# Optimization experiments

Hardware: AMD Instinct MI355X
Metric: run time of the kernel (lower is better)

## Reference

```python
import jax, jax.numpy as jnp
import numpy as np
import math

B, S, D = 2, 2048, 2048
P = 4       # num_entangled_pairs
PW = 2      # num_interference_pathways
L = 2       # num_layers
STD = 0.02
EPS = 1e-5


def _layer_norm(x, g, b):
    m = jnp.mean(x, axis=-1, keepdims=True)
    v = jnp.mean(jnp.square(x - m), axis=-1, keepdims=True)
    return (x - m) * jax.lax.rsqrt(v + EPS) * g + b


def setup_inputs() -> dict:
    key = jax.random.key(0)
    ks = jax.random.split(key, 16)
    n = lambda k, shape: jax.random.normal(k, shape, dtype=jnp.float32) * STD
    inp = {
        "x": jax.random.normal(ks[0], (B, S, D), dtype=jnp.float32),
        # superposition layer
        "amp_w": n(ks[1], (D, D)), "amp_b": jnp.zeros((D,), jnp.float32),
        "ph_w": n(ks[2], (D, D)), "ph_b": jnp.zeros((D,), jnp.float32),
        # per-layer entanglement
        "ent_w": n(ks[3], (L, D, P * D)), "ent_b": jnp.zeros((L, P * D), jnp.float32),
        "ent_pw": n(ks[4], (L, P * D, D)), "ent_pb": jnp.zeros((L, D), jnp.float32),
        # per-layer interference pathways
        "path_w": n(ks[5], (L, PW, D, D)), "path_b": jnp.zeros((L, PW, D), jnp.float32),
        "phase": jax.random.normal(ks[6], (L, PW, D), dtype=jnp.float32),
        # layer norms (norm3 / norm4 of each layer)
        "ln3_g": jnp.ones((L, D), jnp.float32), "ln3_b": jnp.zeros((L, D), jnp.float32),
        "ln4_g": jnp.ones((L, D), jnp.float32), "ln4_b": jnp.zeros((L, D), jnp.float32),
    }
    return inp


def reference(x, amp_w, amp_b, ph_w, ph_b, ent_w, ent_b, ent_pw, ent_pb,
              path_w, path_b, phase, ln3_g, ln3_b, ln4_g, ln4_b):
    # QuantumSuperpositionLayer on the input
    amp = jax.nn.sigmoid(x @ amp_w + amp_b)
    ph = jnp.tanh(x @ ph_w + ph_b) * math.pi
    h = (jnp.cos(ph) + jnp.sin(ph)) * amp                      # [B,S,D]

    for l in range(L):
        # QuantumEntanglementLayer: expand to P*D then project back
        e = h @ ent_w[l] + ent_b[l]                            # [B,S,P*D]
        ent = e @ ent_pw[l] + ent_pb[l]                        # [B,S,D]
        h = _layer_norm(h + ent, ln3_g[l], ln3_b[l])

        # QuantumInterferenceLayer: sum over pathways with phase modulation
        t = jnp.einsum('bsd,pdf->pbsf', h, path_w[l]) + path_b[l][:, None, None, :]
        mod = jnp.cos(phase[l]) + jnp.sin(phase[l])            # [PW,D]
        interf = jnp.sum(t * mod[:, None, None, :], axis=0)   # [B,S,D]
        h = _layer_norm(h + interf, ln4_g[l], ln4_b[l])
    return h
```

## Files before the change

### kernel.cpp

```cpp
#include <hip/hip_runtime.h>
#include <cstdint>
#include <cstddef>

typedef unsigned short u16;
typedef short bf16x8 __attribute__((ext_vector_type(8)));
typedef float f32x4 __attribute__((ext_vector_type(4)));

__device__ __forceinline__ float bf2f(u16 v) {
  union { unsigned int u; float f; } x; x.u = ((unsigned int)v) << 16; return x.f;
}
__device__ __forceinline__ u16 f2bf(float f) {
  union { float f; unsigned int u; } x; x.f = f;
  unsigned int r = (x.u + 0x7fffu + ((x.u >> 16) & 1u)) >> 16;
  return (u16)r;
}

__device__ __forceinline__ void async16(const u16* g, u16* lds) {
  __builtin_amdgcn_global_load_lds(
      (const __attribute__((address_space(1))) void*)g,
      (__attribute__((address_space(3))) void*)lds, 16, 0, 0);
}

#define BM 128
#define BN 128
#define BK 64

__global__ __launch_bounds__(256) void gemm_bt(
    const u16* __restrict__ A, const u16* __restrict__ Bt,
    const float* __restrict__ bias, u16* __restrict__ C,
    int M, int N, int K)
{
  __shared__ __align__(16) u16 As[BM * BK];
  __shared__ __align__(16) u16 Bs[BN * BK];
  const int tid = threadIdx.x;
  const int w   = tid >> 6;
  const int l   = tid & 63;
  const int bm  = blockIdx.x;
  const int bn  = blockIdx.y;
  const int wm  = w >> 1;
  const int wn  = w & 1;
  const int tRow = l & 15;
  const int quad = l >> 4;

  const u16* ag[4]; const u16* bg[4];
  u16* al[4]; u16* bl[4];
  #pragma unroll
  for (int i = 0; i < 4; ++i) {
    int s = i * 4 + w;
    int row = s * 8 + (l >> 3);
    ag[i] = A  + (size_t)(bm * BM + row) * K + (l & 7) * 8;
    bg[i] = Bt + (size_t)(bn * BN + row) * K + (l & 7) * 8;
    al[i] = &As[s * 512];
    bl[i] = &Bs[s * 512];
  }

  f32x4 acc[4][4] = {};

  for (int k0 = 0; k0 < K; k0 += BK) {
    __syncthreads();
    #pragma unroll
    for (int i = 0; i < 4; ++i) {
      async16(ag[i], al[i]);
      async16(bg[i], bl[i]);
      ag[i] += BK; bg[i] += BK;
    }
    __syncthreads();
    #pragma unroll
    for (int ks = 0; ks < BK; ks += 32) {
      bf16x8 af[4], bfr[4];
      #pragma unroll
      for (int mt = 0; mt < 4; ++mt)
        af[mt] = *(const bf16x8*)&As[(wm * 64 + mt * 16 + tRow) * BK + ks + quad * 8];
      #pragma unroll
      for (int nt = 0; nt < 4; ++nt)
        bfr[nt] = *(const bf16x8*)&Bs[(wn * 64 + nt * 16 + tRow) * BK + ks + quad * 8];
      #pragma unroll
      for (int mt = 0; mt < 4; ++mt)
        #pragma unroll
        for (int nt = 0; nt < 4; ++nt)
          acc[mt][nt] = __builtin_amdgcn_mfma_f32_16x16x32_bf16(af[mt], bfr[nt], acc[mt][nt], 0, 0, 0);
    }
  }

  const int crow0 = bm * BM + wm * 64;
  const int ccol0 = bn * BN + wn * 64;
  #pragma unroll
  for (int nt = 0; nt < 4; ++nt) {
    int col = ccol0 + nt * 16 + tRow;
    float bv = bias[col];
    #pragma unroll
    for (int mt = 0; mt < 4; ++mt) {
      int r0 = crow0 + mt * 16 + quad * 4;
      #pragma unroll
      for (int r = 0; r < 4; ++r)
        C[(size_t)(r0 + r) * N + col] = f2bf(acc[mt][nt][r] + bv);
    }
  }
}

__global__ __launch_bounds__(256) void transpose_f2bf(
    const float* __restrict__ src, u16* __restrict__ dst, int R, int C)
{
  __shared__ __align__(16) u16 tile[64][72];
  const int bx = blockIdx.x;
  const int by = blockIdx.y;
  const int t = threadIdx.x;
  const int r  = t >> 4;
  const int c4 = (t & 15) * 4;
  #pragma unroll
  for (int i = 0; i < 4; ++i) {
    int row = r + i * 16;
    f32x4 v = *(const f32x4*)&src[(size_t)(by * 64 + row) * C + bx * 64 + c4];
    #pragma unroll
    for (int j = 0; j < 4; ++j) tile[row][c4 + j] = f2bf(v[j]);
  }
  __syncthreads();
  const int orow0 = t >> 3;
  const int oc8   = (t & 7) * 8;
  #pragma unroll
  for (int i = 0; i < 2; ++i) {
    int orow = orow0 + i * 32;
    u16 tmp[8];
    #pragma unroll
    for (int j = 0; j < 8; ++j) tmp[j] = tile[oc8 + j][orow];
    *(uint4*)&dst[(size_t)(bx * 64 + orow) * R + by * 64 + oc8] = *(uint4*)tmp;
  }
}

__global__ void cvt_f2bf(const float* __restrict__ s, u16* __restrict__ d) {
  size_t i = ((size_t)blockIdx.x * 256 + threadIdx.x) * 8;
  f32x4 a = *(const f32x4*)&s[i];
  f32x4 b = *(const f32x4*)&s[i + 4];
  u16 o[8];
  #pragma unroll
  for (int j = 0; j < 4; ++j) { o[j] = f2bf(a[j]); o[j + 4] = f2bf(b[j]); }
  *(uint4*)&d[i] = *(uint4*)o;
}

__global__ void mod_k(const float* __restrict__ ph, float* __restrict__ m, int n) {
  int i = blockIdx.x * 256 + threadIdx.x;
  if (i < n) { float p = ph[i]; m[i] = cosf(p) + sinf(p); }
}

__global__ __launch_bounds__(256) void combine_path_k(
    const float* __restrict__ pw, const float* __restrict__ mod,
    u16* __restrict__ WcT, int D)
{
  __shared__ float tile[64][65];
  const int bx = blockIdx.x;
  const int by = blockIdx.y;
  const int t = threadIdx.x;
  const int r  = t >> 4;
  const int c4 = (t & 15) * 4;
  float acc[4][4];
  #pragma unroll
  for (int i = 0; i < 4; ++i)
    #pragma unroll
    for (int j = 0; j < 4; ++j) acc[i][j] = 0.f;
  for (int p = 0; p < 2; ++p) {
    float m[4];
    #pragma unroll
    for (int j = 0; j < 4; ++j) m[j] = mod[p * D + bx * 64 + c4 + j];
    #pragma unroll
    for (int i = 0; i < 4; ++i) {
      int d = by * 64 + r + i * 16;
      f32x4 v = *(const f32x4*)&pw[((size_t)p * D + d) * D + bx * 64 + c4];
      #pragma unroll
      for (int j = 0; j < 4; ++j) acc[i][j] += v[j] * m[j];
    }
  }
  #pragma unroll
  for (int i = 0; i < 4; ++i)
    #pragma unroll
    for (int j = 0; j < 4; ++j) tile[r + i * 16][c4 + j] = acc[i][j];
  __syncthreads();
  const int fo0 = t >> 3;
  const int oc8 = (t & 7) * 8;
  #pragma unroll
  for (int i = 0; i < 2; ++i) {
    int fo = fo0 + i * 32;
    u16 tmp[8];
    #pragma unroll
    for (int j = 0; j < 8; ++j) tmp[j] = f2bf(tile[oc8 + j][fo]);
    *(uint4*)&WcT[(size_t)(bx * 64 + fo) * D + by * 64 + oc8] = *(uint4*)tmp;
  }
}

__global__ void combine_bias_k(const float* __restrict__ pb, const float* __restrict__ mod,
                               float* __restrict__ bc, int D) {
  int f = blockIdx.x * 256 + threadIdx.x;
  if (f < D) bc[f] = pb[f] * mod[f] + pb[D + f] * mod[D + f];
}

__global__ __launch_bounds__(256) void superpose_k(
    const u16* __restrict__ z1, const u16* __restrict__ z2, u16* __restrict__ h)
{
  size_t i = ((size_t)blockIdx.x * 256 + threadIdx.x) * 8;
  uint4 v1 = *(const uint4*)&z1[i];
  uint4 v2 = *(const uint4*)&z2[i];
  const u16* p1 = (const u16*)&v1;
  const u16* p2 = (const u16*)&v2;
  u16 o[8];
  #pragma unroll
  for (int j = 0; j < 8; ++j) {
    float a = bf2f(p1[j]);
    float p = bf2f(p2[j]);
    float amp = 1.f / (1.f + __expf(-a));
    float ph = 3.14159265358979323f * tanhf(p);
    float s, c;
    __sincosf(ph, &s, &c);
    o[j] = f2bf((c + s) * amp);
  }
  *(uint4*)&h[i] = *(uint4*)o;
}

template <bool F32OUT>
__global__ __launch_bounds__(256) void add_ln_k(
    const u16* __restrict__ hin, const u16* __restrict__ delta,
    const float* __restrict__ g, const float* __restrict__ b,
    void* __restrict__ outp, int D)
{
  const int row = blockIdx.x;
  const int t = threadIdx.x;
  const size_t base = (size_t)row * D;
  uint4 hv = *(const uint4*)&hin[base + t * 8];
  uint4 dv = *(const uint4*)&delta[base + t * 8];
  const u16* hp = (const u16*)&hv;
  const u16* dp = (const u16*)&dv;
  float x[8];
  float s = 0.f, s2 = 0.f;
  #pragma unroll
  for (int j = 0; j < 8; ++j) {
    x[j] = bf2f(hp[j]) + bf2f(dp[j]);
    s += x[j]; s2 += x[j] * x[j];
  }
  #pragma unroll
  for (int o = 32; o > 0; o >>= 1) {
    s  += __shfl_down(s, o, 64);
    s2 += __shfl_down(s2, o, 64);
  }
  __shared__ float ss[4], ss2[4];
  if ((t & 63) == 0) { ss[t >> 6] = s; ss2[t >> 6] = s2; }
  __syncthreads();
  float S  = ss[0] + ss[1] + ss[2] + ss[3];
  float S2 = ss2[0] + ss2[1] + ss2[2] + ss2[3];
  float mean = S / D;
  float var = S2 / D - mean * mean;
  float rstd = rsqrtf(var + 1e-5f);
  float y[8];
  #pragma unroll
  for (int j = 0; j < 8; ++j)
    y[j] = (x[j] - mean) * rstd * g[t * 8 + j] + b[t * 8 + j];
  if constexpr (F32OUT) {
    float* out = (float*)outp;
    f32x4 lo = {y[0], y[1], y[2], y[3]};
    f32x4 hi = {y[4], y[5], y[6], y[7]};
    *(f32x4*)&out[base + t * 8]     = lo;
    *(f32x4*)&out[base + t * 8 + 4] = hi;
  } else {
    u16* out = (u16*)outp;
    u16 o8[8];
    #pragma unroll
    for (int j = 0; j < 8; ++j) o8[j] = f2bf(y[j]);
    *(uint4*)&out[base + t * 8] = *(uint4*)o8;
  }
}

extern "C" void kernel_launch(void* const* d_in, const int* in_sizes, int n_in,
                              void* d_out, int out_size, void* d_ws, size_t ws_size,
                              hipStream_t stream) {
  const float* x      = (const float*)d_in[0];
  const float* amp_w  = (const float*)d_in[1];
  const float* amp_b  = (const float*)d_in[2];
  const float* ph_w   = (const float*)d_in[3];
  const float* ph_b   = (const float*)d_in[4];
  const float* ent_w  = (const float*)d_in[5];
  const float* ent_b  = (const float*)d_in[6];
  const float* ent_pw = (const float*)d_in[7];
  const float* ent_pb = (const float*)d_in[8];
  const float* path_w = (const float*)d_in[9];
  const float* path_b = (const float*)d_in[10];
  const float* phase  = (const float*)d_in[11];
  const float* ln3_g  = (const float*)d_in[12];
  const float* ln3_b  = (const float*)d_in[13];
  const float* ln4_g  = (const float*)d_in[14];
  const float* ln4_b  = (const float*)d_in[15];

  constexpr int D = 2048, PD = 8192, M = 4096, L = 2, PW = 2;

  char* p = (char*)d_ws;
  u16* wT = (u16*)p; p += (size_t)PD * D * sizeof(u16);
  u16* h  = (u16*)p; p += (size_t)M * D * sizeof(u16);
  u16* t1 = (u16*)p; p += (size_t)M * D * sizeof(u16);
  u16* e  = (u16*)p; p += (size_t)M * PD * sizeof(u16);
  float* modf = (float*)p; p += (size_t)L * PW * D * sizeof(float);
  float* bcf  = (float*)p; p += (size_t)D * sizeof(float);

  u16* xb = e;
  u16* z1 = e + (size_t)M * D;
  u16* z2 = e + (size_t)2 * M * D;

  dim3 b256(256);

  mod_k<<<(L * PW * D) / 256, b256, 0, stream>>>(phase, modf, L * PW * D);
  cvt_f2bf<<<(M * D) / (256 * 8), b256, 0, stream>>>(x, xb);

  transpose_f2bf<<<dim3(D / 64, D / 64), b256, 0, stream>>>(amp_w, wT, D, D);
  gemm_bt<<<dim3(M / BM, D / BN), b256, 0, stream>>>(xb, wT, amp_b, z1, M, D, D);
  transpose_f2bf<<<dim3(D / 64, D / 64), b256, 0, stream>>>(ph_w, wT, D, D);
  gemm_bt<<<dim3(M / BM, D / BN), b256, 0, stream>>>(xb, wT, ph_b, z2, M, D, D);
  superpose_k<<<(M * D) / (256 * 8), b256, 0, stream>>>(z1, z2, h);

  for (int l = 0; l < L; ++l) {
    transpose_f2bf<<<dim3(PD / 64, D / 64), b256, 0, stream>>>(ent_w + (size_t)l * D * PD, wT, D, PD);
    gemm_bt<<<dim3(M / BM, PD / BN), b256, 0, stream>>>(h, wT, ent_b + (size_t)l * PD, e, M, PD, D);
    transpose_f2bf<<<dim3(D / 64, PD / 64), b256, 0, stream>>>(ent_pw + (size_t)l * PD * D, wT, PD, D);
    gemm_bt<<<dim3(M / BM, D / BN), b256, 0, stream>>>(e, wT, ent_pb + (size_t)l * D, t1, M, D, PD);
    add_ln_k<false><<<M, b256, 0, stream>>>(h, t1, ln3_g + (size_t)l * D, ln3_b + (size_t)l * D, h, D);
    combine_path_k<<<dim3(D / 64, D / 64), b256, 0, stream>>>(
        path_w + (size_t)l * PW * D * D, modf + (size_t)l * PW * D, wT, D);
    combine_bias_k<<<D / 256, b256, 0, stream>>>(path_b + (size_t)l * PW * D, modf + (size_t)l * PW * D, bcf, D);
    gemm_bt<<<dim3(M / BM, D / BN), b256, 0, stream>>>(h, wT, bcf, t1, M, D, D);
    if (l == L - 1)
      add_ln_k<true><<<M, b256, 0, stream>>>(h, t1, ln4_g + (size_t)l * D, ln4_b + (size_t)l * D, d_out, D);
    else
      add_ln_k<false><<<M, b256, 0, stream>>>(h, t1, ln4_g + (size_t)l * D, ln4_b + (size_t)l * D, h, D);
  }
}
```

Before: 1.402 ms.

## Swizzle GEMM LDS layout, fuse amp/phase GEMMs, split entanglement weights

Adds an XOR swizzle to the LDS tile layout in the GEMM so the MFMA fragment reads avoid bank conflicts. Merges the amplitude and phase projections into one wider GEMM with concatenated weights and biases. Splits the entanglement expand and project GEMMs into halves so the transposed weight buffer is half as large, with the second projection half accumulating into the bf16 output. The split adds launches and a bf16 read-modify-write accumulation step, which costs some precision.

```diff
diff --git a/kernel.cpp b/kernel.cpp
--- a/kernel.cpp
+++ b/kernel.cpp
@@ -25,9 +25,12 @@
 #define BN 128
 #define BK 64
 
+template <bool ACC>
 __global__ __launch_bounds__(256) void gemm_bt(
-    const u16* __restrict__ A, const u16* __restrict__ Bt,
-    const float* __restrict__ bias, u16* __restrict__ C,
+    const u16* __restrict__ A, int lda,
+    const u16* __restrict__ Bt,
+    const float* __restrict__ bias,
+    u16* __restrict__ C, int ldc,
     int M, int N, int K)
 {
   __shared__ __align__(16) u16 As[BM * BK];
@@ -48,8 +51,9 @@
   for (int i = 0; i < 4; ++i) {
     int s = i * 4 + w;
     int row = s * 8 + (l >> 3);
-    ag[i] = A  + (size_t)(bm * BM + row) * K + (l & 7) * 8;
-    bg[i] = Bt + (size_t)(bn * BN + row) * K + (l & 7) * 8;
+    int c   = (l & 7) ^ ((l >> 3) & 7);
+    ag[i] = A  + (size_t)(bm * BM + row) * lda + c * 8;
+    bg[i] = Bt + (size_t)(bn * BN + row) * K   + c * 8;
     al[i] = &As[s * 512];
     bl[i] = &Bs[s * 512];
   }
@@ -67,13 +71,20 @@
     __syncthreads();
     #pragma unroll
     for (int ks = 0; ks < BK; ks += 32) {
+      const int lc = (ks >> 3) + quad;
       bf16x8 af[4], bfr[4];
       #pragma unroll
-      for (int mt = 0; mt < 4; ++mt)
-        af[mt] = *(const bf16x8*)&As[(wm * 64 + mt * 16 + tRow) * BK + ks + quad * 8];
-      #pragma unroll
-      for (int nt = 0; nt < 4; ++nt)
-        bfr[nt] = *(const bf16x8*)&Bs[(wn * 64 + nt * 16 + tRow) * BK + ks + quad * 8];
+      for (int mt = 0; mt < 4; ++mt) {
+        int r = wm * 64 + mt * 16 + tRow;
+        int p = lc ^ (tRow & 7);
+        af[mt] = *(const bf16x8*)&As[r * BK + p * 8];
+      }
+      #pragma unroll
+      for (int nt = 0; nt < 4; ++nt) {
+        int r = wn * 64 + nt * 16 + tRow;
+        int p = lc ^ (tRow & 7);
+        bfr[nt] = *(const bf16x8*)&Bs[r * BK + p * 8];
+      }
       #pragma unroll
       for (int mt = 0; mt < 4; ++mt)
         #pragma unroll
@@ -87,19 +98,24 @@
   #pragma unroll
   for (int nt = 0; nt < 4; ++nt) {
     int col = ccol0 + nt * 16 + tRow;
-    float bv = bias[col];
+    float bv = ACC ? 0.f : bias[col];
     #pragma unroll
     for (int mt = 0; mt < 4; ++mt) {
       int r0 = crow0 + mt * 16 + quad * 4;
       #pragma unroll
-      for (int r = 0; r < 4; ++r)
-        C[(size_t)(r0 + r) * N + col] = f2bf(acc[mt][nt][r] + bv);
+      for (int r = 0; r < 4; ++r) {
+        size_t idx = (size_t)(r0 + r) * ldc + col;
+        float v = acc[mt][nt][r] + bv;
+        if (ACC) v += bf2f(C[idx]);
+        C[idx] = f2bf(v);
+      }
     }
   }
 }
 
 __global__ __launch_bounds__(256) void transpose_f2bf(
-    const float* __restrict__ src, u16* __restrict__ dst, int R, int C)
+    const float* __restrict__ src, u16* __restrict__ dst,
+    int R, int C, int srcStride, int col0)
 {
   __shared__ __align__(16) u16 tile[64][72];
   const int bx = blockIdx.x;
@@ -110,7 +126,7 @@
   #pragma unroll
   for (int i = 0; i < 4; ++i) {
     int row = r + i * 16;
-    f32x4 v = *(const f32x4*)&src[(size_t)(by * 64 + row) * C + bx * 64 + c4];
+    f32x4 v = *(const f32x4*)&src[(size_t)(by * 64 + row) * srcStride + col0 + bx * 64 + c4];
     #pragma unroll
     for (int j = 0; j < 4; ++j) tile[row][c4 + j] = f2bf(v[j]);
   }
@@ -140,6 +156,12 @@
 __global__ void mod_k(const float* __restrict__ ph, float* __restrict__ m, int n) {
   int i = blockIdx.x * 256 + threadIdx.x;
   if (i < n) { float p = ph[i]; m[i] = cosf(p) + sinf(p); }
+}
+
+__global__ void concat2_k(const float* __restrict__ a, const float* __restrict__ b,
+                          float* __restrict__ d, int n) {
+  int i = blockIdx.x * 256 + threadIdx.x;
+  if (i < n) { d[i] = a[i]; d[n + i] = b[i]; }
 }
 
 __global__ __launch_bounds__(256) void combine_path_k(
@@ -193,11 +215,15 @@
 }
 
 __global__ __launch_bounds__(256) void superpose_k(
-    const u16* __restrict__ z1, const u16* __restrict__ z2, u16* __restrict__ h)
-{
-  size_t i = ((size_t)blockIdx.x * 256 + threadIdx.x) * 8;
-  uint4 v1 = *(const uint4*)&z1[i];
-  uint4 v2 = *(const uint4*)&z2[i];
+    const u16* __restrict__ zc, u16* __restrict__ h, int D)
+{
+  size_t idx = (size_t)blockIdx.x * 256 + threadIdx.x;
+  int grpPerRow = D / 8;
+  size_t row = idx / grpPerRow;
+  int cg = (int)(idx % grpPerRow);
+  size_t zbase = row * (size_t)(2 * D) + cg * 8;
+  uint4 v1 = *(const uint4*)&zc[zbase];
+  uint4 v2 = *(const uint4*)&zc[zbase + D];
   const u16* p1 = (const u16*)&v1;
   const u16* p2 = (const u16*)&v2;
   u16 o[8];
@@ -211,7 +237,7 @@
     __sincosf(ph, &s, &c);
     o[j] = f2bf((c + s) * amp);
   }
-  *(uint4*)&h[i] = *(uint4*)o;
+  *(uint4*)&h[row * D + cg * 8] = *(uint4*)o;
 }
 
 template <bool F32OUT>
@@ -287,40 +313,55 @@
   const float* ln4_b  = (const float*)d_in[15];
 
   constexpr int D = 2048, PD = 8192, M = 4096, L = 2, PW = 2;
+  constexpr int HPD = PD / 2;
 
   char* p = (char*)d_ws;
-  u16* wT = (u16*)p; p += (size_t)PD * D * sizeof(u16);
+  float* modf = (float*)p; p += (size_t)L * PW * D * sizeof(float);
+  float* bcf  = (float*)p; p += (size_t)2 * D * sizeof(float);
+  p = (char*)d_ws + 65536;
   u16* h  = (u16*)p; p += (size_t)M * D * sizeof(u16);
   u16* t1 = (u16*)p; p += (size_t)M * D * sizeof(u16);
+  u16* wT = (u16*)p; p += (size_t)HPD * D * sizeof(u16);
   u16* e  = (u16*)p; p += (size_t)M * PD * sizeof(u16);
-  float* modf = (float*)p; p += (size_t)L * PW * D * sizeof(float);
-  float* bcf  = (float*)p; p += (size_t)D * sizeof(float);
 
   u16* xb = e;
-  u16* z1 = e + (size_t)M * D;
-  u16* z2 = e + (size_t)2 * M * D;
+  u16* zc = e + (size_t)M * D;
 
   dim3 b256(256);
 
   mod_k<<<(L * PW * D) / 256, b256, 0, stream>>>(phase, modf, L * PW * D);
   cvt_f2bf<<<(M * D) / (256 * 8), b256, 0, stream>>>(x, xb);
 
-  transpose_f2bf<<<dim3(D / 64, D / 64), b256, 0, stream>>>(amp_w, wT, D, D);
-  gemm_bt<<<dim3(M / BM, D / BN), b256, 0, stream>>>(xb, wT, amp_b, z1, M, D, D);
-  transpose_f2bf<<<dim3(D / 64, D / 64), b256, 0, stream>>>(ph_w, wT, D, D);
-  gemm_bt<<<dim3(M / BM, D / BN), b256, 0, stream>>>(xb, wT, ph_b, z2, M, D, D);
-  superpose_k<<<(M * D) / (256 * 8), b256, 0, stream>>>(z1, z2, h);
+  transpose_f2bf<<<dim3(D / 64, D / 64), b256, 0, stream>>>(amp_w, wT, D, D, D, 0);
+  transpose_f2bf<<<dim3(D / 64, D / 64), b256, 0, stream>>>(ph_w, wT + (size_t)D * D, D, D, D, 0);
+  concat2_k<<<D / 256, b256, 0, stream>>>(amp_b, ph_b, bcf, D);
+  gemm_bt<false><<<dim3(M / BM, (2 * D) / BN), b256, 0, stream>>>(
+      xb, D, wT, bcf, zc, 2 * D, M, 2 * D, D);
+  superpose_k<<<(M * D) / (256 * 8), b256, 0, stream>>>(zc, h, D);
 
   for (int l = 0; l < L; ++l) {
-    transpose_f2bf<<<dim3(PD / 64, D / 64), b256, 0, stream>>>(ent_w + (size_t)l * D * PD, wT, D, PD);
-    gemm_bt<<<dim3(M / BM, PD / BN), b256, 0, stream>>>(h, wT, ent_b + (size_t)l * PD, e, M, PD, D);
-    transpose_f2bf<<<dim3(D / 64, PD / 64), b256, 0, stream>>>(ent_pw + (size_t)l * PD * D, wT, PD, D);
-    gemm_bt<<<dim3(M / BM, D / BN), b256, 0, stream>>>(e, wT, ent_pb + (size_t)l * D, t1, M, D, PD);
+    for (int s = 0; s < 2; ++s) {
+      transpose_f2bf<<<dim3(HPD / 64, D / 64), b256, 0, stream>>>(
+          ent_w + (size_t)l * D * PD, wT, D, HPD, PD, s * HPD);
+      gemm_bt<false><<<dim3(M / BM, HPD / BN), b256, 0, stream>>>(
+          h, D, wT, ent_b + (size_t)l * PD + s * HPD, e + s * HPD, PD, M, HPD, D);
+    }
+    for (int s = 0; s < 2; ++s) {
+      transpose_f2bf<<<dim3(D / 64, HPD / 64), b256, 0, stream>>>(
+          ent_pw + (size_t)l * PD * D + (size_t)s * HPD * D, wT, HPD, D, D, 0);
+      if (s == 0)
+        gemm_bt<false><<<dim3(M / BM, D / BN), b256, 0, stream>>>(
+            e, PD, wT, ent_pb + (size_t)l * D, t1, D, M, D, HPD);
+      else
+        gemm_bt<true><<<dim3(M / BM, D / BN), b256, 0, stream>>>(
+            e + HPD, PD, wT, bcf , t1, D, M, D, HPD);
+    }
     add_ln_k<false><<<M, b256, 0, stream>>>(h, t1, ln3_g + (size_t)l * D, ln3_b + (size_t)l * D, h, D);
     combine_path_k<<<dim3(D / 64, D / 64), b256, 0, stream>>>(
         path_w + (size_t)l * PW * D * D, modf + (size_t)l * PW * D, wT, D);
     combine_bias_k<<<D / 256, b256, 0, stream>>>(path_b + (size_t)l * PW * D, modf + (size_t)l * PW * D, bcf, D);
-    gemm_bt<<<dim3(M / BM, D / BN), b256, 0, stream>>>(h, wT, bcf, t1, M, D, D);
+    gemm_bt<false><<<dim3(M / BM, D / BN), b256, 0, stream>>>(
+        h, D, wT, bcf, t1, D, M, D, D);
     if (l == L - 1)
       add_ln_k<true><<<M, b256, 0, stream>>>(h, t1, ln4_g + (size_t)l * D, ln4_b + (size_t)l * D, d_out, D);
     else
```

Result: faster. 1.293 ms (-7.7%).
